# Kernel optimization log

Measured on AMD Instinct MI355X. Metric: run time of the kernel, lower is better.

The kernel has to match this reference:

```python
import jax, jax.numpy as jnp
import numpy as np

N, E, D, H, G = 50000, 800000, 256, 256, 64
EPS = 1e-5

def setup_inputs() -> dict:
    key = jax.random.key(0)
    ks = jax.random.split(key, 16)
    s_in = float(np.sqrt(2.0 / D))   # He fan_in init
    s_h = float(np.sqrt(2.0 / H))
    inp = {}
    inp['x'] = jax.random.normal(ks[0], (N, D), jnp.float32)
    inp['edge_index'] = jax.random.randint(ks[1], (2, E), 0, N)
    inp['batch'] = jnp.sort(jax.random.randint(ks[2], (N,), 0, G))
    inp['bn_in_g'] = jnp.ones((D,), jnp.float32)
    inp['bn_in_b'] = jnp.zeros((D,), jnp.float32)
    for i in range(3):
        fan = D if i == 0 else H
        inp[f'W{i}'] = jax.random.normal(ks[3 + i], (fan, H), jnp.float32) * float(np.sqrt(2.0 / fan))
        inp[f'b{i}'] = jnp.zeros((H,), jnp.float32)
        inp[f'bn{i}_g'] = jnp.ones((H,), jnp.float32)
        inp[f'bn{i}_b'] = jnp.zeros((H,), jnp.float32)
    inp['Wa1'] = jax.random.normal(ks[6], (H, H // 2), jnp.float32) * s_h
    inp['ba1'] = jnp.zeros((H // 2,), jnp.float32)
    inp['Wa2'] = jax.random.normal(ks[7], (H // 2, 1), jnp.float32) * float(np.sqrt(2.0 / (H // 2)))
    inp['ba2'] = jnp.zeros((1,), jnp.float32)
    inp['Wo'] = jax.random.normal(ks[8], (H, 2), jnp.float32) * s_h
    inp['bo'] = jnp.zeros((2,), jnp.float32)
    return inp


def _bn(x, g, b):
    # BatchNorm1d, batch statistics (training-mode normalization), biased var
    m = jnp.mean(x, axis=0)
    v = jnp.mean(jnp.square(x - m), axis=0)
    return (x - m) * jax.lax.rsqrt(v + EPS) * g + b


def _gcn(x, src, dst, W, b):
    h = x @ W  # [N, H]
    n = x.shape[0]
    deg = jax.ops.segment_sum(jnp.ones_like(src, x.dtype), dst, num_segments=n) + 1.0  # +1 self-loop
    dinv = jax.lax.rsqrt(deg)  # [N]
    msg = h[src] * (dinv[src] * dinv[dst])[:, None]          # gather + edgewise scale
    agg = jax.ops.segment_sum(msg, dst, num_segments=n)      # scatter-add at dst
    return agg + h * (dinv * dinv)[:, None] + b               # self-loop term fused


def reference(x, edge_index, batch, bn_in_g, bn_in_b,
              W0, b0, bn0_g, bn0_b, W1, b1, bn1_g, bn1_b, W2, b2, bn2_g, bn2_b,
              Wa1, ba1, Wa2, ba2, Wo, bo):
    src, dst = edge_index[0], edge_index[1]
    x = _bn(x, bn_in_g, bn_in_b)  # dropout = identity (eval)
    # layer 0
    xp = _bn(jax.nn.relu(_gcn(x, src, dst, W0, b0)), bn0_g, bn0_b)
    # layers 1..2 with residual
    for (W, b, g, bb) in ((W1, b1, bn1_g, bn1_b), (W2, b2, bn2_g, bn2_b)):
        xn = _bn(jax.nn.relu(_gcn(xp, src, dst, W, b)), g, bb)
        xp = xn + xp
    # attention over all nodes (softmax along node dim, as in source)
    scores = jax.nn.leaky_relu(xp @ Wa1 + ba1, 0.01) @ Wa2 + ba2  # [N,1]
    w = jax.nn.softmax(scores, axis=0)
    xw = xp * w
    cnt = jax.ops.segment_sum(jnp.ones((xp.shape[0],), xp.dtype), batch, num_segments=G)
    pooled = jax.ops.segment_sum(xw, batch, num_segments=G) / jnp.maximum(cnt, 1.0)[:, None]
    return pooled @ Wo + bo  # [G, 2]
```

## Files before the change

kernel.cpp:

```cpp
#include <hip/hip_runtime.h>

#define N_NODES 50000
#define N_EDGES 800000
#define DIM 256
#define NG 64
#define EPS_BN 1e-5f

typedef _Float16 f16;
typedef _Float16 half8 __attribute__((ext_vector_type(8)));
typedef _Float16 half4 __attribute__((ext_vector_type(4)));
typedef float floatx4 __attribute__((ext_vector_type(4)));

__global__ __launch_bounds__(256) void col_stats_kernel(const float* __restrict__ X, int n,
                                                        float* __restrict__ sums, int relu) {
    int c = threadIdx.x;
    float s = 0.f, q = 0.f;
    for (int i = blockIdx.x; i < n; i += gridDim.x) {
        float v = X[(size_t)i * DIM + c];
        if (relu) v = fmaxf(v, 0.f);
        s += v; q += v * v;
    }
    atomicAdd(&sums[c], s);
    atomicAdd(&sums[DIM + c], q);
}

__global__ void finalize_stats_kernel(const float* __restrict__ sums, float* __restrict__ mr, float inv_n) {
    int c = threadIdx.x;
    float m = sums[c] * inv_n;
    float v = sums[DIM + c] * inv_n - m * m;
    mr[c] = m;
    mr[DIM + c] = rsqrtf(v + EPS_BN);
}

__global__ __launch_bounds__(256) void bn_apply_kernel(const float* __restrict__ Cin, f16* __restrict__ Af,
                                                       const float* __restrict__ mr, const float* __restrict__ g,
                                                       const float* __restrict__ b, int n, int relu, int residual) {
    int c = threadIdx.x;
    float mean = mr[c], rstd = mr[DIM + c], gg = g[c], bb = b[c];
    for (int i = blockIdx.x; i < n; i += gridDim.x) {
        size_t idx = (size_t)i * DIM + c;
        float v = Cin[idx];
        if (relu) v = fmaxf(v, 0.f);
        v = (v - mean) * rstd * gg + bb;
        if (residual) v += (float)Af[idx];
        Af[idx] = (f16)v;
    }
}

__global__ void convert_wT_kernel(const float* __restrict__ W, f16* __restrict__ Wt, int K, int M) {
    int idx = blockIdx.x * 256 + threadIdx.x;
    if (idx < K * M) {
        int m = idx / K, k = idx % K;
        Wt[idx] = (f16)W[(size_t)k * M + m];
    }
}

__global__ void count_int_kernel(const int* __restrict__ idx, int n, int* __restrict__ cnt) {
    for (int i = blockIdx.x * blockDim.x + threadIdx.x; i < n; i += gridDim.x * blockDim.x)
        atomicAdd(&cnt[idx[i]], 1);
}

__global__ void dinv_kernel(const int* __restrict__ cnt, float* __restrict__ dinv, int n) {
    for (int i = blockIdx.x * blockDim.x + threadIdx.x; i < n; i += gridDim.x * blockDim.x)
        dinv[i] = rsqrtf((float)cnt[i] + 1.0f);
}

#define SCHUNK 2048
__global__ __launch_bounds__(256) void scan1_kernel(const int* __restrict__ cnt, int n,
                                                    int* __restrict__ outp, int* __restrict__ bsums) {
    __shared__ int lds[256];
    int t = threadIdx.x;
    int base = blockIdx.x * SCHUNK + t * 8;
    int v[8]; int s = 0;
#pragma unroll
    for (int j = 0; j < 8; j++) { int id = base + j; int x = (id < n) ? cnt[id] : 0; v[j] = s; s += x; }
    lds[t] = s; __syncthreads();
    for (int o = 1; o < 256; o <<= 1) {
        int add = (t >= o) ? lds[t - o] : 0;
        __syncthreads();
        lds[t] += add;
        __syncthreads();
    }
    int excl = lds[t] - s;
#pragma unroll
    for (int j = 0; j < 8; j++) { int id = base + j; if (id < n) outp[id] = excl + v[j]; }
    if (t == 255) bsums[blockIdx.x] = lds[255];
}

__global__ void scan2_kernel(int* bsums, int nb) {
    if (threadIdx.x == 0 && blockIdx.x == 0) {
        int r = 0;
        for (int i = 0; i < nb; i++) { int t = bsums[i]; bsums[i] = r; r += t; }
    }
}

__global__ void scan3_kernel(int* __restrict__ outp, const int* __restrict__ bsums, int n, int total) {
    int i = blockIdx.x * blockDim.x + threadIdx.x;
    if (i < n) outp[i] += bsums[i / SCHUNK];
    if (i == 0) outp[n] = total;
}

__global__ void scatter_kernel(const int* __restrict__ src, const int* __restrict__ dst, int ne,
                               const int* __restrict__ rowp, int* __restrict__ fill, int* __restrict__ ss) {
    for (int e = blockIdx.x * blockDim.x + threadIdx.x; e < ne; e += gridDim.x * blockDim.x) {
        int d = dst[e];
        int pos = rowp[d] + atomicAdd(&fill[d], 1);
        ss[pos] = src[e];
    }
}

__global__ void graph_bounds_kernel(const int* __restrict__ batch, int n, int* __restrict__ start) {
    int i = blockIdx.x * blockDim.x + threadIdx.x;
    if (i < n) {
        int b = batch[i];
        if (i == 0 || batch[i - 1] != b) start[b] = i;
    }
}

__global__ void graph_offsets2_kernel(const int* __restrict__ start, int* __restrict__ off, int* __restrict__ cnt) {
    if (threadIdx.x == 0 && blockIdx.x == 0) {
        int nxt = N_NODES;
        for (int g = NG - 1; g >= 0; --g) {
            int s = start[g];
            int o = (s < 0) ? nxt : s;
            off[g] = o;
            cnt[g] = nxt - o;
            nxt = o;
        }
    }
}

__global__ __launch_bounds__(256) void gcn_agg_kernel(const f16* __restrict__ h, const int* __restrict__ rowp,
                                                      const int* __restrict__ ss, const float* __restrict__ dinv,
                                                      const float* __restrict__ bias, float* __restrict__ out, int n) {
    int wave = threadIdx.x >> 6;
    int lane = threadIdx.x & 63;
    int row = blockIdx.x * 4 + wave;
    if (row >= n) return;
    int c = lane * 4;
    float ax = 0.f, ay = 0.f, az = 0.f, aw = 0.f;
    int e0 = rowp[row], e1 = rowp[row + 1];
    int e = e0;
    for (; e + 3 < e1; e += 4) {
        int s0 = ss[e], s1 = ss[e + 1], s2 = ss[e + 2], s3 = ss[e + 3];
        float w0 = dinv[s0], w1 = dinv[s1], w2 = dinv[s2], w3 = dinv[s3];
        half4 h0 = *(const half4*)&h[(size_t)s0 * DIM + c];
        half4 h1 = *(const half4*)&h[(size_t)s1 * DIM + c];
        half4 h2 = *(const half4*)&h[(size_t)s2 * DIM + c];
        half4 h3 = *(const half4*)&h[(size_t)s3 * DIM + c];
        ax += w0 * (float)h0[0] + w1 * (float)h1[0] + w2 * (float)h2[0] + w3 * (float)h3[0];
        ay += w0 * (float)h0[1] + w1 * (float)h1[1] + w2 * (float)h2[1] + w3 * (float)h3[1];
        az += w0 * (float)h0[2] + w1 * (float)h1[2] + w2 * (float)h2[2] + w3 * (float)h3[2];
        aw += w0 * (float)h0[3] + w1 * (float)h1[3] + w2 * (float)h2[3] + w3 * (float)h3[3];
    }
    for (; e < e1; e++) {
        int s = ss[e];
        float w = dinv[s];
        half4 hv = *(const half4*)&h[(size_t)s * DIM + c];
        ax += w * (float)hv[0]; ay += w * (float)hv[1]; az += w * (float)hv[2]; aw += w * (float)hv[3];
    }
    float di = dinv[row];
    float d2 = di * di;
    half4 hs = *(const half4*)&h[(size_t)row * DIM + c];
    float4 bv = *(const float4*)&bias[c];
    float4 r;
    r.x = di * ax + d2 * (float)hs[0] + bv.x;
    r.y = di * ay + d2 * (float)hs[1] + bv.y;
    r.z = di * az + d2 * (float)hs[2] + bv.z;
    r.w = di * aw + d2 * (float)hs[3] + bv.w;
    *(float4*)&out[(size_t)row * DIM + c] = r;
}

#define BM 128
#define BN 128
#define BK 32
#define LDP 40
__global__ __launch_bounds__(256) void gemm_f16_kernel(const f16* __restrict__ Af, const f16* __restrict__ Wt,
                                                       f16* __restrict__ C, int n, int K, int M) {
    __shared__ __align__(16) f16 As[BM * LDP];
    __shared__ __align__(16) f16 Bs[BN * LDP];
    int tid = threadIdx.x;
    int wave = tid >> 6, lane = tid & 63;
    int wm = wave >> 1, wn = wave & 1;
    int q = lane >> 4, l16 = lane & 15;
    int bm = blockIdx.x * BM, bn = blockIdx.y * BN;
    floatx4 acc[4][4] = {};
    for (int k0 = 0; k0 < K; k0 += BK) {
#pragma unroll
        for (int rr = 0; rr < 2; rr++) {
            int cidx = tid + rr * 256;
            int row = cidx >> 2, off = (cidx & 3) * 8;
            int arow = bm + row; if (arow >= n) arow = n - 1;
            *(float4*)&As[row * LDP + off] = *(const float4*)&Af[(size_t)arow * K + k0 + off];
            int brow = bn + row;
            *(float4*)&Bs[row * LDP + off] = *(const float4*)&Wt[(size_t)brow * K + k0 + off];
        }
        __syncthreads();
        half8 af[4], bf[4];
#pragma unroll
        for (int i = 0; i < 4; i++) af[i] = *(half8*)&As[(wm * 64 + i * 16 + l16) * LDP + q * 8];
#pragma unroll
        for (int j = 0; j < 4; j++) bf[j] = *(half8*)&Bs[(wn * 64 + j * 16 + l16) * LDP + q * 8];
#pragma unroll
        for (int i = 0; i < 4; i++)
#pragma unroll
            for (int j = 0; j < 4; j++)
                acc[i][j] = __builtin_amdgcn_mfma_f32_16x16x32_f16(af[i], bf[j], acc[i][j], 0, 0, 0);
        __syncthreads();
    }
#pragma unroll
    for (int i = 0; i < 4; i++)
#pragma unroll
        for (int j = 0; j < 4; j++) {
            int col = bn + wn * 64 + j * 16 + l16;
#pragma unroll
            for (int r = 0; r < 4; r++) {
                int row = bm + wm * 64 + i * 16 + q * 4 + r;
                if (row < n) C[(size_t)row * M + col] = (f16)acc[i][j][r];
            }
        }
}

__global__ __launch_bounds__(256) void attn_score_kernel(const f16* __restrict__ T, const float* __restrict__ ba1,
                                                         const float* __restrict__ Wa2, const float* __restrict__ ba2,
                                                         float* __restrict__ score, int n) {
    int wave = threadIdx.x >> 6, lane = threadIdx.x & 63;
    int row = blockIdx.x * 4 + wave;
    if (row >= n) return;
    float s = 0.f;
#pragma unroll
    for (int j = lane; j < 128; j += 64) {
        float v = (float)T[(size_t)row * 128 + j] + ba1[j];
        v = (v > 0.f) ? v : 0.01f * v;
        s += v * Wa2[j];
    }
    for (int o = 32; o > 0; o >>= 1) s += __shfl_down(s, o);
    if (lane == 0) score[row] = s + ba2[0];
}

__global__ __launch_bounds__(256) void reduce_max_kernel(const float* __restrict__ s, int n, float* __restrict__ part) {
    __shared__ float lds[256];
    float m = -3.0e38f;
    for (int i = blockIdx.x * 256 + threadIdx.x; i < n; i += gridDim.x * 256) m = fmaxf(m, s[i]);
    lds[threadIdx.x] = m; __syncthreads();
    for (int o = 128; o > 0; o >>= 1) {
        if (threadIdx.x < o) lds[threadIdx.x] = fmaxf(lds[threadIdx.x], lds[threadIdx.x + o]);
        __syncthreads();
    }
    if (threadIdx.x == 0) part[blockIdx.x] = lds[0];
}

__global__ void reduce_max_final_kernel(const float* __restrict__ part, int nb, float* __restrict__ red) {
    __shared__ float lds[256];
    float m = -3.0e38f;
    for (int i = threadIdx.x; i < nb; i += 256) m = fmaxf(m, part[i]);
    lds[threadIdx.x] = m; __syncthreads();
    for (int o = 128; o > 0; o >>= 1) {
        if (threadIdx.x < o) lds[threadIdx.x] = fmaxf(lds[threadIdx.x], lds[threadIdx.x + o]);
        __syncthreads();
    }
    if (threadIdx.x == 0) red[0] = lds[0];
}

__global__ __launch_bounds__(256) void reduce_sumexp_kernel(const float* __restrict__ s, int n,
                                                            const float* __restrict__ red, float* __restrict__ part) {
    __shared__ float lds[256];
    float mx = red[0];
    float acc = 0.f;
    for (int i = blockIdx.x * 256 + threadIdx.x; i < n; i += gridDim.x * 256) acc += expf(s[i] - mx);
    lds[threadIdx.x] = acc; __syncthreads();
    for (int o = 128; o > 0; o >>= 1) {
        if (threadIdx.x < o) lds[threadIdx.x] += lds[threadIdx.x + o];
        __syncthreads();
    }
    if (threadIdx.x == 0) part[blockIdx.x] = lds[0];
}

__global__ void reduce_sum_final_kernel(const float* __restrict__ part, int nb, float* __restrict__ red) {
    __shared__ float lds[256];
    float s = 0.f;
    for (int i = threadIdx.x; i < nb; i += 256) s += part[i];
    lds[threadIdx.x] = s; __syncthreads();
    for (int o = 128; o > 0; o >>= 1) {
        if (threadIdx.x < o) lds[threadIdx.x] += lds[threadIdx.x + o];
        __syncthreads();
    }
    if (threadIdx.x == 0) red[1] = lds[0];
}

__global__ __launch_bounds__(256) void pool_kernel(const f16* __restrict__ Af, const float* __restrict__ score,
                                                   const int* __restrict__ offs, const int* __restrict__ cnts,
                                                   const float* __restrict__ red, float* __restrict__ pooled) {
    int g = blockIdx.x, c = threadIdx.x;
    int st = offs[g], cn = cnts[g];
    float mx = red[0];
    float acc = 0.f;
    for (int i = (int)blockIdx.y; i < cn; i += 32) {
        int i1 = i + 8, i2 = i + 16, i3 = i + 24;
        float s0 = score[st + i];
        float s1 = (i1 < cn) ? score[st + i1] : -3.0e38f;
        float s2 = (i2 < cn) ? score[st + i2] : -3.0e38f;
        float s3 = (i3 < cn) ? score[st + i3] : -3.0e38f;
        float a0 = (float)Af[(size_t)(st + i) * DIM + c];
        float a1 = (i1 < cn) ? (float)Af[(size_t)(st + i1) * DIM + c] : 0.f;
        float a2 = (i2 < cn) ? (float)Af[(size_t)(st + i2) * DIM + c] : 0.f;
        float a3 = (i3 < cn) ? (float)Af[(size_t)(st + i3) * DIM + c] : 0.f;
        acc += a0 * expf(s0 - mx) + a1 * expf(s1 - mx) + a2 * expf(s2 - mx) + a3 * expf(s3 - mx);
    }
    atomicAdd(&pooled[g * DIM + c], acc);
}

__global__ __launch_bounds__(256) void out_kernel(const float* __restrict__ pooled, const int* __restrict__ cnt,
                                                  const float* __restrict__ red, const float* __restrict__ Wo,
                                                  const float* __restrict__ bo, float* __restrict__ out) {
    __shared__ float l0[256], l1[256];
    int g = blockIdx.x, c = threadIdx.x;
    float scale = 1.f / (red[1] * fmaxf((float)cnt[g], 1.f));
    float v = pooled[g * DIM + c] * scale;
    l0[c] = v * Wo[c * 2];
    l1[c] = v * Wo[c * 2 + 1];
    __syncthreads();
    for (int o = 128; o > 0; o >>= 1) {
        if (c < o) { l0[c] += l0[c + o]; l1[c] += l1[c + o]; }
        __syncthreads();
    }
    if (c == 0) { out[g * 2] = l0[0] + bo[0]; out[g * 2 + 1] = l1[0] + bo[1]; }
}

extern "C" void kernel_launch(void* const* d_in, const int* in_sizes, int n_in,
                              void* d_out, int out_size, void* d_ws, size_t ws_size,
                              hipStream_t stream) {
    const float* x       = (const float*)d_in[0];
    const int*   ei      = (const int*)d_in[1];
    const int*   batch   = (const int*)d_in[2];
    const float* bn_in_g = (const float*)d_in[3];
    const float* bn_in_b = (const float*)d_in[4];
    const float* Ws[3]   = {(const float*)d_in[5],  (const float*)d_in[9],  (const float*)d_in[13]};
    const float* bs[3]   = {(const float*)d_in[6],  (const float*)d_in[10], (const float*)d_in[14]};
    const float* gs[3]   = {(const float*)d_in[7],  (const float*)d_in[11], (const float*)d_in[15]};
    const float* bbs[3]  = {(const float*)d_in[8],  (const float*)d_in[12], (const float*)d_in[16]};
    const float* Wa1 = (const float*)d_in[17];
    const float* ba1 = (const float*)d_in[18];
    const float* Wa2 = (const float*)d_in[19];
    const float* ba2 = (const float*)d_in[20];
    const float* Wo  = (const float*)d_in[21];
    const float* bo  = (const float*)d_in[22];

    char* w = (char*)d_ws;
    size_t off = 0;
    auto alloc = [&](size_t bytes) -> void* {
        void* p = w + off;
        off += (bytes + 255) & ~(size_t)255;
        return p;
    };
    f16*   Afh  = (f16*)alloc((size_t)N_NODES * DIM * 2);
    f16*   Bh   = (f16*)alloc((size_t)N_NODES * DIM * 2);
    float* C    = (float*)alloc((size_t)N_NODES * DIM * 4);
    f16*   Wt[3];
    for (int l = 0; l < 3; l++) Wt[l] = (f16*)alloc((size_t)DIM * DIM * 2);
    f16*   Wa1t = (f16*)alloc((size_t)128 * DIM * 2);
    int* sorted_src = (int*)alloc((size_t)N_EDGES * 4);
    int* deg    = (int*)alloc((size_t)N_NODES * 4);
    float* dinv = (float*)alloc((size_t)N_NODES * 4);
    int* rowp   = (int*)alloc((size_t)(N_NODES + 1) * 4);
    int* fill   = (int*)alloc((size_t)N_NODES * 4);
    float* score = (float*)alloc((size_t)N_NODES * 4);
    float* stats = (float*)alloc(512 * 4);
    float* mr    = (float*)alloc(512 * 4);
    int* bsums   = (int*)alloc(64 * 4);
    float* part  = (float*)alloc(256 * 4);
    float* red   = (float*)alloc(16 * 4);
    int* gstart  = (int*)alloc(64 * 4);
    int* cnt_g   = (int*)alloc(64 * 4);
    int* off_g   = (int*)alloc(64 * 4);
    float* pooled = (float*)alloc((size_t)NG * DIM * 4);

    const int* src = ei;
    const int* dst = ei + N_EDGES;

    hipMemsetAsync(deg, 0, (size_t)N_NODES * 4, stream);
    hipMemsetAsync(fill, 0, (size_t)N_NODES * 4, stream);
    count_int_kernel<<<3125, 256, 0, stream>>>(dst, N_EDGES, deg);
    dinv_kernel<<<196, 256, 0, stream>>>(deg, dinv, N_NODES);
    scan1_kernel<<<(N_NODES + SCHUNK - 1) / SCHUNK, 256, 0, stream>>>(deg, N_NODES, rowp, bsums);
    scan2_kernel<<<1, 64, 0, stream>>>(bsums, (N_NODES + SCHUNK - 1) / SCHUNK);
    scan3_kernel<<<(N_NODES + 255) / 256, 256, 0, stream>>>(rowp, bsums, N_NODES, N_EDGES);
    scatter_kernel<<<3125, 256, 0, stream>>>(src, dst, N_EDGES, rowp, fill, sorted_src);

    hipMemsetAsync(gstart, 0xff, 64 * 4, stream);
    graph_bounds_kernel<<<(N_NODES + 255) / 256, 256, 0, stream>>>(batch, N_NODES, gstart);
    graph_offsets2_kernel<<<1, 64, 0, stream>>>(gstart, off_g, cnt_g);

    for (int l = 0; l < 3; l++)
        convert_wT_kernel<<<DIM * DIM / 256, 256, 0, stream>>>(Ws[l], Wt[l], DIM, DIM);
    convert_wT_kernel<<<128 * DIM / 256, 256, 0, stream>>>(Wa1, Wa1t, DIM, 128);

    hipMemsetAsync(stats, 0, 512 * 4, stream);
    col_stats_kernel<<<512, 256, 0, stream>>>(x, N_NODES, stats, 0);
    finalize_stats_kernel<<<1, 256, 0, stream>>>(stats, mr, 1.f / N_NODES);
    bn_apply_kernel<<<1024, 256, 0, stream>>>(x, Afh, mr, bn_in_g, bn_in_b, N_NODES, 0, 0);

    dim3 ggrid((N_NODES + BM - 1) / BM, DIM / BN);
    for (int l = 0; l < 3; l++) {
        gemm_f16_kernel<<<ggrid, 256, 0, stream>>>(Afh, Wt[l], Bh, N_NODES, DIM, DIM);
        gcn_agg_kernel<<<(N_NODES + 3) / 4, 256, 0, stream>>>(Bh, rowp, sorted_src, dinv, bs[l], C, N_NODES);
        hipMemsetAsync(stats, 0, 512 * 4, stream);
        col_stats_kernel<<<512, 256, 0, stream>>>(C, N_NODES, stats, 1);
        finalize_stats_kernel<<<1, 256, 0, stream>>>(stats, mr, 1.f / N_NODES);
        bn_apply_kernel<<<1024, 256, 0, stream>>>(C, Afh, mr, gs[l], bbs[l], N_NODES, 1, (l > 0) ? 1 : 0);
    }

    dim3 agrid((N_NODES + BM - 1) / BM, 1);
    gemm_f16_kernel<<<agrid, 256, 0, stream>>>(Afh, Wa1t, Bh, N_NODES, DIM, 128);
    attn_score_kernel<<<(N_NODES + 3) / 4, 256, 0, stream>>>(Bh, ba1, Wa2, ba2, score, N_NODES);
    reduce_max_kernel<<<256, 256, 0, stream>>>(score, N_NODES, part);
    reduce_max_final_kernel<<<1, 256, 0, stream>>>(part, 256, red);
    reduce_sumexp_kernel<<<256, 256, 0, stream>>>(score, N_NODES, red, part);
    reduce_sum_final_kernel<<<1, 256, 0, stream>>>(part, 256, red);

    hipMemsetAsync(pooled, 0, (size_t)NG * DIM * 4, stream);
    pool_kernel<<<dim3(NG, 8), 256, 0, stream>>>(Afh, score, off_g, cnt_g, red, pooled);
    out_kernel<<<NG, 256, 0, stream>>>(pooled, cnt_g, red, Wo, bo, (float*)d_out);
}
```

Before: 831.4 us.

## Fuse BN stats into aggregation, attention score into GEMM, and trim launches

```diff
diff --git a/kernel.cpp b/kernel.cpp
--- a/kernel.cpp
+++ b/kernel.cpp
@@ -12,12 +12,11 @@
 typedef float floatx4 __attribute__((ext_vector_type(4)));
 
 __global__ __launch_bounds__(256) void col_stats_kernel(const float* __restrict__ X, int n,
-                                                        float* __restrict__ sums, int relu) {
+                                                        float* __restrict__ sums) {
     int c = threadIdx.x;
     float s = 0.f, q = 0.f;
     for (int i = blockIdx.x; i < n; i += gridDim.x) {
         float v = X[(size_t)i * DIM + c];
-        if (relu) v = fmaxf(v, 0.f);
         s += v; q += v * v;
     }
     atomicAdd(&sums[c], s);
@@ -32,15 +31,28 @@
     mr[DIM + c] = rsqrtf(v + EPS_BN);
 }
 
-__global__ __launch_bounds__(256) void bn_apply_kernel(const float* __restrict__ Cin, f16* __restrict__ Af,
-                                                       const float* __restrict__ mr, const float* __restrict__ g,
-                                                       const float* __restrict__ b, int n, int relu, int residual) {
+__global__ __launch_bounds__(256) void bn_apply_in_kernel(const float* __restrict__ Xin, f16* __restrict__ Af,
+                                                          const float* __restrict__ mr, const float* __restrict__ g,
+                                                          const float* __restrict__ b, int n) {
     int c = threadIdx.x;
     float mean = mr[c], rstd = mr[DIM + c], gg = g[c], bb = b[c];
     for (int i = blockIdx.x; i < n; i += gridDim.x) {
         size_t idx = (size_t)i * DIM + c;
-        float v = Cin[idx];
-        if (relu) v = fmaxf(v, 0.f);
+        float v = Xin[idx];
+        v = (v - mean) * rstd * gg + bb;
+        Af[idx] = (f16)v;
+    }
+}
+
+__global__ __launch_bounds__(256) void bn_apply_kernel(const f16* __restrict__ Cin, f16* __restrict__ Af,
+                                                       const float* __restrict__ mr, const float* __restrict__ g,
+                                                       const float* __restrict__ b, int n, int residual) {
+    int c = threadIdx.x;
+    float mean = mr[c], rstd = mr[DIM + c], gg = g[c], bb = b[c];
+    for (int i = blockIdx.x; i < n; i += gridDim.x) {
+        size_t idx = (size_t)i * DIM + c;
+        float v = (float)Cin[idx];
+        v = fmaxf(v, 0.f);
         v = (v - mean) * rstd * gg + bb;
         if (residual) v += (float)Af[idx];
         Af[idx] = (f16)v;
@@ -60,20 +72,21 @@
         atomicAdd(&cnt[idx[i]], 1);
 }
 
-__global__ void dinv_kernel(const int* __restrict__ cnt, float* __restrict__ dinv, int n) {
-    for (int i = blockIdx.x * blockDim.x + threadIdx.x; i < n; i += gridDim.x * blockDim.x)
-        dinv[i] = rsqrtf((float)cnt[i] + 1.0f);
-}
-
 #define SCHUNK 2048
 __global__ __launch_bounds__(256) void scan1_kernel(const int* __restrict__ cnt, int n,
-                                                    int* __restrict__ outp, int* __restrict__ bsums) {
+                                                    int* __restrict__ outp, int* __restrict__ bsums,
+                                                    float* __restrict__ dinv) {
     __shared__ int lds[256];
     int t = threadIdx.x;
     int base = blockIdx.x * SCHUNK + t * 8;
     int v[8]; int s = 0;
 #pragma unroll
-    for (int j = 0; j < 8; j++) { int id = base + j; int x = (id < n) ? cnt[id] : 0; v[j] = s; s += x; }
+    for (int j = 0; j < 8; j++) {
+        int id = base + j;
+        int x = 0;
+        if (id < n) { x = cnt[id]; dinv[id] = rsqrtf((float)x + 1.0f); }
+        v[j] = s; s += x;
+    }
     lds[t] = s; __syncthreads();
     for (int o = 1; o < 256; o <<= 1) {
         int add = (t >= o) ? lds[t - o] : 0;
@@ -132,43 +145,69 @@
 
 __global__ __launch_bounds__(256) void gcn_agg_kernel(const f16* __restrict__ h, const int* __restrict__ rowp,
                                                       const int* __restrict__ ss, const float* __restrict__ dinv,
-                                                      const float* __restrict__ bias, float* __restrict__ out, int n) {
+                                                      const float* __restrict__ bias, f16* __restrict__ out,
+                                                      float* __restrict__ stats, int n) {
     int wave = threadIdx.x >> 6;
     int lane = threadIdx.x & 63;
-    int row = blockIdx.x * 4 + wave;
-    if (row >= n) return;
     int c = lane * 4;
-    float ax = 0.f, ay = 0.f, az = 0.f, aw = 0.f;
-    int e0 = rowp[row], e1 = rowp[row + 1];
-    int e = e0;
-    for (; e + 3 < e1; e += 4) {
-        int s0 = ss[e], s1 = ss[e + 1], s2 = ss[e + 2], s3 = ss[e + 3];
-        float w0 = dinv[s0], w1 = dinv[s1], w2 = dinv[s2], w3 = dinv[s3];
-        half4 h0 = *(const half4*)&h[(size_t)s0 * DIM + c];
-        half4 h1 = *(const half4*)&h[(size_t)s1 * DIM + c];
-        half4 h2 = *(const half4*)&h[(size_t)s2 * DIM + c];
-        half4 h3 = *(const half4*)&h[(size_t)s3 * DIM + c];
-        ax += w0 * (float)h0[0] + w1 * (float)h1[0] + w2 * (float)h2[0] + w3 * (float)h3[0];
-        ay += w0 * (float)h0[1] + w1 * (float)h1[1] + w2 * (float)h2[1] + w3 * (float)h3[1];
-        az += w0 * (float)h0[2] + w1 * (float)h1[2] + w2 * (float)h2[2] + w3 * (float)h3[2];
-        aw += w0 * (float)h0[3] + w1 * (float)h1[3] + w2 * (float)h2[3] + w3 * (float)h3[3];
-    }
-    for (; e < e1; e++) {
-        int s = ss[e];
-        float w = dinv[s];
-        half4 hv = *(const half4*)&h[(size_t)s * DIM + c];
-        ax += w * (float)hv[0]; ay += w * (float)hv[1]; az += w * (float)hv[2]; aw += w * (float)hv[3];
-    }
-    float di = dinv[row];
-    float d2 = di * di;
-    half4 hs = *(const half4*)&h[(size_t)row * DIM + c];
     float4 bv = *(const float4*)&bias[c];
-    float4 r;
-    r.x = di * ax + d2 * (float)hs[0] + bv.x;
-    r.y = di * ay + d2 * (float)hs[1] + bv.y;
-    r.z = di * az + d2 * (float)hs[2] + bv.z;
-    r.w = di * aw + d2 * (float)hs[3] + bv.w;
-    *(float4*)&out[(size_t)row * DIM + c] = r;
+    float s0 = 0.f, s1 = 0.f, s2 = 0.f, s3 = 0.f;
+    float q0 = 0.f, q1 = 0.f, q2 = 0.f, q3 = 0.f;
+    for (int row = blockIdx.x * 4 + wave; row < n; row += gridDim.x * 4) {
+        float ax = 0.f, ay = 0.f, az = 0.f, aw = 0.f;
+        int e0 = rowp[row], e1 = rowp[row + 1];
+        int e = e0;
+        for (; e + 3 < e1; e += 4) {
+            int i0 = ss[e], i1 = ss[e + 1], i2 = ss[e + 2], i3 = ss[e + 3];
+            float w0 = dinv[i0], w1 = dinv[i1], w2 = dinv[i2], w3 = dinv[i3];
+            half4 h0 = *(const half4*)&h[(size_t)i0 * DIM + c];
+            half4 h1 = *(const half4*)&h[(size_t)i1 * DIM + c];
+            half4 h2 = *(const half4*)&h[(size_t)i2 * DIM + c];
+            half4 h3 = *(const half4*)&h[(size_t)i3 * DIM + c];
+            ax += w0 * (float)h0[0] + w1 * (float)h1[0] + w2 * (float)h2[0] + w3 * (float)h3[0];
+            ay += w0 * (float)h0[1] + w1 * (float)h1[1] + w2 * (float)h2[1] + w3 * (float)h3[1];
+            az += w0 * (float)h0[2] + w1 * (float)h1[2] + w2 * (float)h2[2] + w3 * (float)h3[2];
+            aw += w0 * (float)h0[3] + w1 * (float)h1[3] + w2 * (float)h2[3] + w3 * (float)h3[3];
+        }
+        for (; e < e1; e++) {
+            int si = ss[e];
+            float ww = dinv[si];
+            half4 hv = *(const half4*)&h[(size_t)si * DIM + c];
+            ax += ww * (float)hv[0]; ay += ww * (float)hv[1];
+            az += ww * (float)hv[2]; aw += ww * (float)hv[3];
+        }
+        float di = dinv[row];
+        float d2 = di * di;
+        half4 hs = *(const half4*)&h[(size_t)row * DIM + c];
+        float rx = di * ax + d2 * (float)hs[0] + bv.x;
+        float ry = di * ay + d2 * (float)hs[1] + bv.y;
+        float rz = di * az + d2 * (float)hs[2] + bv.z;
+        float rw = di * aw + d2 * (float)hs[3] + bv.w;
+        half4 o; o[0] = (f16)rx; o[1] = (f16)ry; o[2] = (f16)rz; o[3] = (f16)rw;
+        *(half4*)&out[(size_t)row * DIM + c] = o;
+        float t;
+        t = fmaxf(rx, 0.f); s0 += t; q0 += t * t;
+        t = fmaxf(ry, 0.f); s1 += t; q1 += t * t;
+        t = fmaxf(rz, 0.f); s2 += t; q2 += t * t;
+        t = fmaxf(rw, 0.f); s3 += t; q3 += t * t;
+    }
+    __shared__ float sred[4][64][4];
+    __shared__ float qred[4][64][4];
+    sred[wave][lane][0] = s0; sred[wave][lane][1] = s1; sred[wave][lane][2] = s2; sred[wave][lane][3] = s3;
+    qred[wave][lane][0] = q0; qred[wave][lane][1] = q1; qred[wave][lane][2] = q2; qred[wave][lane][3] = q3;
+    __syncthreads();
+    if (wave == 0) {
+        float a0 = 0.f, a1 = 0.f, a2 = 0.f, a3 = 0.f, b0 = 0.f, b1 = 0.f, b2 = 0.f, b3 = 0.f;
+#pragma unroll
+        for (int ww = 0; ww < 4; ww++) {
+            a0 += sred[ww][lane][0]; a1 += sred[ww][lane][1]; a2 += sred[ww][lane][2]; a3 += sred[ww][lane][3];
+            b0 += qred[ww][lane][0]; b1 += qred[ww][lane][1]; b2 += qred[ww][lane][2]; b3 += qred[ww][lane][3];
+        }
+        atomicAdd(&stats[c + 0], a0); atomicAdd(&stats[c + 1], a1);
+        atomicAdd(&stats[c + 2], a2); atomicAdd(&stats[c + 3], a3);
+        atomicAdd(&stats[DIM + c + 0], b0); atomicAdd(&stats[DIM + c + 1], b1);
+        atomicAdd(&stats[DIM + c + 2], b2); atomicAdd(&stats[DIM + c + 3], b3);
+    }
 }
 
 #define BM 128
@@ -221,21 +260,68 @@
         }
 }
 
-__global__ __launch_bounds__(256) void attn_score_kernel(const f16* __restrict__ T, const float* __restrict__ ba1,
-                                                         const float* __restrict__ Wa2, const float* __restrict__ ba2,
-                                                         float* __restrict__ score, int n) {
-    int wave = threadIdx.x >> 6, lane = threadIdx.x & 63;
-    int row = blockIdx.x * 4 + wave;
-    if (row >= n) return;
-    float s = 0.f;
-#pragma unroll
-    for (int j = lane; j < 128; j += 64) {
-        float v = (float)T[(size_t)row * 128 + j] + ba1[j];
-        v = (v > 0.f) ? v : 0.01f * v;
-        s += v * Wa2[j];
-    }
-    for (int o = 32; o > 0; o >>= 1) s += __shfl_down(s, o);
-    if (lane == 0) score[row] = s + ba2[0];
+__global__ __launch_bounds__(256) void gemm_attn_kernel(const f16* __restrict__ Af, const f16* __restrict__ Wt,
+                                                        const float* __restrict__ ba1, const float* __restrict__ Wa2,
+                                                        const float* __restrict__ ba2, float* __restrict__ score,
+                                                        int n, int K) {
+    __shared__ __align__(16) f16 As[BM * LDP];
+    __shared__ __align__(16) f16 Bs[128 * LDP];
+    __shared__ float scred[128][2];
+    int tid = threadIdx.x;
+    int wave = tid >> 6, lane = tid & 63;
+    int wm = wave >> 1, wn = wave & 1;
+    int q = lane >> 4, l16 = lane & 15;
+    int bm = blockIdx.x * BM;
+    floatx4 acc[4][4] = {};
+    for (int k0 = 0; k0 < K; k0 += BK) {
+#pragma unroll
+        for (int rr = 0; rr < 2; rr++) {
+            int cidx = tid + rr * 256;
+            int row = cidx >> 2, off = (cidx & 3) * 8;
+            int arow = bm + row; if (arow >= n) arow = n - 1;
+            *(float4*)&As[row * LDP + off] = *(const float4*)&Af[(size_t)arow * K + k0 + off];
+            *(float4*)&Bs[row * LDP + off] = *(const float4*)&Wt[(size_t)row * K + k0 + off];
+        }
+        __syncthreads();
+        half8 af[4], bf[4];
+#pragma unroll
+        for (int i = 0; i < 4; i++) af[i] = *(half8*)&As[(wm * 64 + i * 16 + l16) * LDP + q * 8];
+#pragma unroll
+        for (int j = 0; j < 4; j++) bf[j] = *(half8*)&Bs[(wn * 64 + j * 16 + l16) * LDP + q * 8];
+#pragma unroll
+        for (int i = 0; i < 4; i++)
+#pragma unroll
+            for (int j = 0; j < 4; j++)
+                acc[i][j] = __builtin_amdgcn_mfma_f32_16x16x32_f16(af[i], bf[j], acc[i][j], 0, 0, 0);
+        __syncthreads();
+    }
+    float ba1v[4], wa2v[4];
+#pragma unroll
+    for (int j = 0; j < 4; j++) {
+        int col = wn * 64 + j * 16 + l16;
+        ba1v[j] = ba1[col];
+        wa2v[j] = Wa2[col];
+    }
+#pragma unroll
+    for (int i = 0; i < 4; i++)
+#pragma unroll
+        for (int r = 0; r < 4; r++) {
+            float p = 0.f;
+#pragma unroll
+            for (int j = 0; j < 4; j++) {
+                float v = acc[i][j][r] + ba1v[j];
+                v = (v > 0.f) ? v : 0.01f * v;
+                p += v * wa2v[j];
+            }
+#pragma unroll
+            for (int o = 1; o < 16; o <<= 1) p += __shfl_xor(p, o);
+            if (l16 == 0) scred[wm * 64 + i * 16 + q * 4 + r][wn] = p;
+        }
+    __syncthreads();
+    if (tid < 128) {
+        int grow = bm + tid;
+        if (grow < n) score[grow] = scred[tid][0] + scred[tid][1] + ba2[0];
+    }
 }
 
 __global__ __launch_bounds__(256) void reduce_max_kernel(const float* __restrict__ s, int n, float* __restrict__ part) {
@@ -250,50 +336,41 @@
     if (threadIdx.x == 0) part[blockIdx.x] = lds[0];
 }
 
-__global__ void reduce_max_final_kernel(const float* __restrict__ part, int nb, float* __restrict__ red) {
+__global__ __launch_bounds__(256) void reduce_sumexp_kernel(const float* __restrict__ s, int n,
+                                                            const float* __restrict__ part_max,
+                                                            float* __restrict__ part_sum) {
     __shared__ float lds[256];
-    float m = -3.0e38f;
-    for (int i = threadIdx.x; i < nb; i += 256) m = fmaxf(m, part[i]);
-    lds[threadIdx.x] = m; __syncthreads();
+    int t = threadIdx.x;
+    lds[t] = part_max[t]; __syncthreads();
     for (int o = 128; o > 0; o >>= 1) {
-        if (threadIdx.x < o) lds[threadIdx.x] = fmaxf(lds[threadIdx.x], lds[threadIdx.x + o]);
-        __syncthreads();
-    }
-    if (threadIdx.x == 0) red[0] = lds[0];
-}
-
-__global__ __launch_bounds__(256) void reduce_sumexp_kernel(const float* __restrict__ s, int n,
-                                                            const float* __restrict__ red, float* __restrict__ part) {
-    __shared__ float lds[256];
-    float mx = red[0];
+        if (t < o) lds[t] = fmaxf(lds[t], lds[t + o]);
+        __syncthreads();
+    }
+    float mx = lds[0];
+    __syncthreads();
     float acc = 0.f;
-    for (int i = blockIdx.x * 256 + threadIdx.x; i < n; i += gridDim.x * 256) acc += expf(s[i] - mx);
-    lds[threadIdx.x] = acc; __syncthreads();
+    for (int i = blockIdx.x * 256 + t; i < n; i += gridDim.x * 256) acc += expf(s[i] - mx);
+    lds[t] = acc; __syncthreads();
     for (int o = 128; o > 0; o >>= 1) {
-        if (threadIdx.x < o) lds[threadIdx.x] += lds[threadIdx.x + o];
-        __syncthreads();
-    }
-    if (threadIdx.x == 0) part[blockIdx.x] = lds[0];
-}
-
-__global__ void reduce_sum_final_kernel(const float* __restrict__ part, int nb, float* __restrict__ red) {
-    __shared__ float lds[256];
-    float s = 0.f;
-    for (int i = threadIdx.x; i < nb; i += 256) s += part[i];
-    lds[threadIdx.x] = s; __syncthreads();
-    for (int o = 128; o > 0; o >>= 1) {
-        if (threadIdx.x < o) lds[threadIdx.x] += lds[threadIdx.x + o];
-        __syncthreads();
-    }
-    if (threadIdx.x == 0) red[1] = lds[0];
+        if (t < o) lds[t] += lds[t + o];
+        __syncthreads();
+    }
+    if (t == 0) part_sum[blockIdx.x] = lds[0];
 }
 
 __global__ __launch_bounds__(256) void pool_kernel(const f16* __restrict__ Af, const float* __restrict__ score,
                                                    const int* __restrict__ offs, const int* __restrict__ cnts,
-                                                   const float* __restrict__ red, float* __restrict__ pooled) {
-    int g = blockIdx.x, c = threadIdx.x;
+                                                   const float* __restrict__ part_max, float* __restrict__ pooled) {
+    __shared__ float lds[256];
+    int c = threadIdx.x;
+    lds[c] = part_max[c]; __syncthreads();
+    for (int o = 128; o > 0; o >>= 1) {
+        if (c < o) lds[c] = fmaxf(lds[c], lds[c + o]);
+        __syncthreads();
+    }
+    float mx = lds[0];
+    int g = blockIdx.x;
     int st = offs[g], cn = cnts[g];
-    float mx = red[0];
     float acc = 0.f;
     for (int i = (int)blockIdx.y; i < cn; i += 32) {
         int i1 = i + 8, i2 = i + 16, i3 = i + 24;
@@ -311,11 +388,18 @@
 }
 
 __global__ __launch_bounds__(256) void out_kernel(const float* __restrict__ pooled, const int* __restrict__ cnt,
-                                                  const float* __restrict__ red, const float* __restrict__ Wo,
+                                                  const float* __restrict__ part_sum, const float* __restrict__ Wo,
                                                   const float* __restrict__ bo, float* __restrict__ out) {
     __shared__ float l0[256], l1[256];
     int g = blockIdx.x, c = threadIdx.x;
-    float scale = 1.f / (red[1] * fmaxf((float)cnt[g], 1.f));
+    l0[c] = part_sum[c]; __syncthreads();
+    for (int o = 128; o > 0; o >>= 1) {
+        if (c < o) l0[c] += l0[c + o];
+        __syncthreads();
+    }
+    float denom = l0[0];
+    __syncthreads();
+    float scale = 1.f / (denom * fmaxf((float)cnt[g], 1.f));
     float v = pooled[g * DIM + c] * scale;
     l0[c] = v * Wo[c * 2];
     l1[c] = v * Wo[c * 2 + 1];
@@ -353,41 +437,42 @@
         off += (bytes + 255) & ~(size_t)255;
         return p;
     };
+    int*   deg     = (int*)alloc((size_t)N_NODES * 4);
+    int*   fill    = (int*)alloc((size_t)N_NODES * 4);
+    float* statsA  = (float*)alloc(4 * 512 * 4);
+    float* pooled  = (float*)alloc((size_t)NG * DIM * 4);
+    size_t zero_span = off;
     f16*   Afh  = (f16*)alloc((size_t)N_NODES * DIM * 2);
     f16*   Bh   = (f16*)alloc((size_t)N_NODES * DIM * 2);
-    float* C    = (float*)alloc((size_t)N_NODES * DIM * 4);
+    f16*   Ch   = (f16*)alloc((size_t)N_NODES * DIM * 2);
     f16*   Wt[3];
     for (int l = 0; l < 3; l++) Wt[l] = (f16*)alloc((size_t)DIM * DIM * 2);
     f16*   Wa1t = (f16*)alloc((size_t)128 * DIM * 2);
     int* sorted_src = (int*)alloc((size_t)N_EDGES * 4);
-    int* deg    = (int*)alloc((size_t)N_NODES * 4);
     float* dinv = (float*)alloc((size_t)N_NODES * 4);
     int* rowp   = (int*)alloc((size_t)(N_NODES + 1) * 4);
-    int* fill   = (int*)alloc((size_t)N_NODES * 4);
     float* score = (float*)alloc((size_t)N_NODES * 4);
-    float* stats = (float*)alloc(512 * 4);
     float* mr    = (float*)alloc(512 * 4);
     int* bsums   = (int*)alloc(64 * 4);
-    float* part  = (float*)alloc(256 * 4);
-    float* red   = (float*)alloc(16 * 4);
+    float* part_max = (float*)alloc(256 * 4);
+    float* part_sum = (float*)alloc(256 * 4);
     int* gstart  = (int*)alloc(64 * 4);
     int* cnt_g   = (int*)alloc(64 * 4);
     int* off_g   = (int*)alloc(64 * 4);
-    float* pooled = (float*)alloc((size_t)NG * DIM * 4);
 
     const int* src = ei;
     const int* dst = ei + N_EDGES;
-
-    hipMemsetAsync(deg, 0, (size_t)N_NODES * 4, stream);
-    hipMemsetAsync(fill, 0, (size_t)N_NODES * 4, stream);
+    const int NSCAN = (N_NODES + SCHUNK - 1) / SCHUNK;
+
+    hipMemsetAsync(d_ws, 0, zero_span, stream);
+    hipMemsetAsync(gstart, 0xff, 64 * 4, stream);
+
     count_int_kernel<<<3125, 256, 0, stream>>>(dst, N_EDGES, deg);
-    dinv_kernel<<<196, 256, 0, stream>>>(deg, dinv, N_NODES);
-    scan1_kernel<<<(N_NODES + SCHUNK - 1) / SCHUNK, 256, 0, stream>>>(deg, N_NODES, rowp, bsums);
-    scan2_kernel<<<1, 64, 0, stream>>>(bsums, (N_NODES + SCHUNK - 1) / SCHUNK);
+    scan1_kernel<<<NSCAN, 256, 0, stream>>>(deg, N_NODES, rowp, bsums, dinv);
+    scan2_kernel<<<1, 64, 0, stream>>>(bsums, NSCAN);
     scan3_kernel<<<(N_NODES + 255) / 256, 256, 0, stream>>>(rowp, bsums, N_NODES, N_EDGES);
     scatter_kernel<<<3125, 256, 0, stream>>>(src, dst, N_EDGES, rowp, fill, sorted_src);
 
-    hipMemsetAsync(gstart, 0xff, 64 * 4, stream);
     graph_bounds_kernel<<<(N_NODES + 255) / 256, 256, 0, stream>>>(batch, N_NODES, gstart);
     graph_offsets2_kernel<<<1, 64, 0, stream>>>(gstart, off_g, cnt_g);
 
@@ -395,30 +480,23 @@
         convert_wT_kernel<<<DIM * DIM / 256, 256, 0, stream>>>(Ws[l], Wt[l], DIM, DIM);
     convert_wT_kernel<<<128 * DIM / 256, 256, 0, stream>>>(Wa1, Wa1t, DIM, 128);
 
-    hipMemsetAsync(stats, 0, 512 * 4, stream);
-    col_stats_kernel<<<512, 256, 0, stream>>>(x, N_NODES, stats, 0);
-    finalize_stats_kernel<<<1, 256, 0, stream>>>(stats, mr, 1.f / N_NODES);
-    bn_apply_kernel<<<1024, 256, 0, stream>>>(x, Afh, mr, bn_in_g, bn_in_b, N_NODES, 0, 0);
+    col_stats_kernel<<<512, 256, 0, stream>>>(x, N_NODES, statsA);
+    finalize_stats_kernel<<<1, 256, 0, stream>>>(statsA, mr, 1.f / N_NODES);
+    bn_apply_in_kernel<<<1024, 256, 0, stream>>>(x, Afh, mr, bn_in_g, bn_in_b, N_NODES);
 
     dim3 ggrid((N_NODES + BM - 1) / BM, DIM / BN);
     for (int l = 0; l < 3; l++) {
+        float* statsL = statsA + 512 * (l + 1);
         gemm_f16_kernel<<<ggrid, 256, 0, stream>>>(Afh, Wt[l], Bh, N_NODES, DIM, DIM);
-        gcn_agg_kernel<<<(N_NODES + 3) / 4, 256, 0, stream>>>(Bh, rowp, sorted_src, dinv, bs[l], C, N_NODES);
-        hipMemsetAsync(stats, 0, 512 * 4, stream);
-        col_stats_kernel<<<512, 256, 0, stream>>>(C, N_NODES, stats, 1);
-        finalize_stats_kernel<<<1, 256, 0, stream>>>(stats, mr, 1.f / N_NODES);
-        bn_apply_kernel<<<1024, 256, 0, stream>>>(C, Afh, mr, gs[l], bbs[l], N_NODES, 1, (l > 0) ? 1 : 0);
-    }
-
-    dim3 agrid((N_NODES + BM - 1) / BM, 1);
-    gemm_f16_kernel<<<agrid, 256, 0, stream>>>(Afh, Wa1t, Bh, N_NODES, DIM, 128);
-    attn_score_kernel<<<(N_NODES + 3) / 4, 256, 0, stream>>>(Bh, ba1, Wa2, ba2, score, N_NODES);
-    reduce_max_kernel<<<256, 256, 0, stream>>>(score, N_NODES, part);
-    reduce_max_final_kernel<<<1, 256, 0, stream>>>(part, 256, red);
-    reduce_sumexp_kernel<<<256, 256, 0, stream>>>(score, N_NODES, red, part);
-    reduce_sum_final_kernel<<<1, 256, 0, stream>>>(part, 256, red);
-
-    hipMemsetAsync(pooled, 0, (size_t)NG * DIM * 4, stream);
-    pool_kernel<<<dim3(NG, 8), 256, 0, stream>>>(Afh, score, off_g, cnt_g, red, pooled);
-    out_kernel<<<NG, 256, 0, stream>>>(pooled, cnt_g, red, Wo, bo, (float*)d_out);
-}
+        gcn_agg_kernel<<<3125, 256, 0, stream>>>(Bh, rowp, sorted_src, dinv, bs[l], Ch, statsL, N_NODES);
+        finalize_stats_kernel<<<1, 256, 0, stream>>>(statsL, mr, 1.f / N_NODES);
+        bn_apply_kernel<<<1024, 256, 0, stream>>>(Ch, Afh, mr, gs[l], bbs[l], N_NODES, (l > 0) ? 1 : 0);
+    }
+
+    gemm_attn_kernel<<<(N_NODES + BM - 1) / BM, 256, 0, stream>>>(Afh, Wa1t, ba1, Wa2, ba2, score, N_NODES, DIM);
+    reduce_max_kernel<<<256, 256, 0, stream>>>(score, N_NODES, part_max);
+    reduce_sumexp_kernel<<<256, 256, 0, stream>>>(score, N_NODES, part_max, part_sum);
+
+    pool_kernel<<<dim3(NG, 8), 256, 0, stream>>>(Afh, score, off_g, cnt_g, part_max, pooled);
+    out_kernel<<<NG, 256, 0, stream>>>(pooled, cnt_g, part_sum, Wo, bo, (float*)d_out);
+}
```

Result: slower. 1.495 ms (+79.9%).
